# Optimization experiments

Hardware: AMD Instinct MI355X
Metric: run time of the kernel (lower is better)

## Reference

```python
import jax, jax.numpy as jnp
import numpy as np

B, C, T, H, W = 8, 128, 16, 32, 32
M, N, CS = 64, 64, 64


def setup_inputs() -> dict:
    key = jax.random.key(0)
    ks = jax.random.split(key, 12)
    s = 0.02
    return {
        "input": jax.random.normal(ks[0], (B, C, T, H, W), dtype=jnp.float32),
        "condition": jax.random.normal(ks[1], (B, CS), dtype=jnp.float32),
        # 1x1x1 Conv3d weights collapse to (out, in) matrices
        "W_phi": jax.random.normal(ks[2], (M, C), dtype=jnp.float32) * s,
        "b_phi": jax.random.normal(ks[3], (M,), dtype=jnp.float32) * s,
        "W_theta": jax.random.normal(ks[4], (N, C), dtype=jnp.float32) * s,
        "b_theta": jax.random.normal(ks[5], (N,), dtype=jnp.float32) * s,
        "W_rho": jax.random.normal(ks[6], (N, C), dtype=jnp.float32) * s,
        "b_rho": jax.random.normal(ks[7], (N,), dtype=jnp.float32) * s,
        "W1": jax.random.normal(ks[8], (CS, CS), dtype=jnp.float32) * s,
        "b1": jax.random.normal(ks[9], (CS,), dtype=jnp.float32) * s,
        "W2": jax.random.normal(ks[10], (H * W, CS), dtype=jnp.float32) * s,
        "b2": jax.random.normal(ks[11], (H * W,), dtype=jnp.float32) * s,
    }


def _pointwise_conv3d(x, Wt, b):
    # Conv3d with kernel=1, stride=1 == channel mixing
    return jnp.einsum('bcthw,oc->bothw', x, Wt) + b[None, :, None, None, None]


def reference(input, condition, W_phi, b_phi, W_theta, b_theta, W_rho, b_rho, W1, b1, W2, b2):
    x = input.reshape(-1, C, T, H, W)
    cond = condition.reshape(x.shape[0], -1)
    A = _pointwise_conv3d(x, W_phi, b_phi)                       # (b,m,t,h,w)
    B0 = _pointwise_conv3d(x, W_theta, b_theta)                  # (b,n,t,h,w)
    Bm = jax.nn.softmax(B0.reshape(B0.shape[0], B0.shape[1], -1), axis=-1).reshape(B0.shape)
    # FC_Cond: Linear+ReLU, Linear+ReLU, then softmax over h*w
    h1 = jax.nn.relu(cond @ W1.T + b1)
    h2 = jax.nn.relu(h1 @ W2.T + b2)
    Cm = jax.nn.softmax(h2, axis=-1).reshape(-1, H, W)           # (b,h,w)
    BC = Bm * Cm[:, None, None, :, :]                            # (b,n,t,h,w)
    AB_T = jnp.einsum('bmthw,bnthw->bmn', A, BC)                 # (b,m,n)
    V = jax.nn.softmax(_pointwise_conv3d(x, W_rho, b_rho), axis=1)
    Z = jnp.einsum('bmn,bnthw->bmthw', AB_T, V)
    attn = jnp.transpose(Bm * V, (0, 1, 3, 4, 2))                # (b,n,h,w,t)
    return (Z, attn)
```

## Files before the change

### kernel.cpp

```cpp
#include <hip/hip_runtime.h>

#define CC 128
#define SB 16384

typedef _Float16 half2_t __attribute__((ext_vector_type(2)));
typedef _Float16 half4_t __attribute__((ext_vector_type(4)));
typedef _Float16 half8_t __attribute__((ext_vector_type(8)));
typedef float    f32x4  __attribute__((ext_vector_type(4)));

#define WH_OFF   0u
#define ABH_OFF  0u
#define BIAS_OFF 49152u
#define CM_OFF   50176u
#define SUME_OFF 82944u
#define PT_OFF   262144u
#define VT_OFF   33816576u

__global__ void k0_setup(const float* __restrict__ cond,
                         const float* __restrict__ W_phi, const float* __restrict__ b_phi,
                         const float* __restrict__ W_theta, const float* __restrict__ b_theta,
                         const float* __restrict__ W_rho, const float* __restrict__ b_rho,
                         const float* __restrict__ W1, const float* __restrict__ b1,
                         const float* __restrict__ W2, const float* __restrict__ b2,
                         char* __restrict__ wsc) {
  __shared__ float sc[64], sh1[64], red[256];
  int t = threadIdx.x, bid = blockIdx.x;
  if (bid < 8) {
    int b = bid;
    if (t < 64) sc[t] = cond[b*64 + t];
    __syncthreads();
    if (t < 64) {
      float acc = b1[t];
      for (int k = 0; k < 64; ++k) acc += sc[k] * W1[t*64 + k];
      sh1[t] = fmaxf(acc, 0.f);
    }
    __syncthreads();
    float ev[4]; float ps = 0.f;
    #pragma unroll
    for (int q = 0; q < 4; ++q) {
      int o = q*256 + t;
      float acc = b2[o];
      for (int k = 0; k < 64; ++k) acc += sh1[k] * W2[o*64 + k];
      ev[q] = __expf(fmaxf(acc, 0.f));
      ps += ev[q];
    }
    red[t] = ps; __syncthreads();
    for (int s = 128; s > 0; s >>= 1) { if (t < s) red[t] += red[t+s]; __syncthreads(); }
    float inv = 1.f / red[0];
    float* cm = (float*)(wsc + CM_OFF);
    #pragma unroll
    for (int q = 0; q < 4; ++q) cm[b*1024 + q*256 + t] = ev[q] * inv;
  } else {
    int r = bid - 8;
    _Float16* wh = (_Float16*)(wsc + WH_OFF);
    for (int i = r*256 + t; i < 24576; i += 2048) {
      int set = i >> 13, mk = i & 8191;
      const float* W = (set == 0) ? W_phi : (set == 1 ? W_theta : W_rho);
      wh[i] = (_Float16)W[mk];
    }
    if (r == 0 && t < 192) {
      float* bias = (float*)(wsc + BIAS_OFF);
      bias[t] = (t < 64) ? b_phi[t] : (t < 128 ? b_theta[t-64] : b_rho[t-128]);
    }
    if (r == 1) {
      float* se = (float*)(wsc + SUME_OFF);
      for (int i = t; i < 512; i += 256) se[i] = 0.f;
    }
  }
}

__global__ __launch_bounds__(256, 4) void kC_main(
    const float* __restrict__ x, const _Float16* __restrict__ wh,
    const float* __restrict__ bias, const float* __restrict__ cm,
    float* __restrict__ sumE, _Float16* __restrict__ vt,
    char* __restrict__ ptb,
    float* __restrict__ part) {
  __shared__ char smem[35328];
  __shared__ float se_l[256];
  _Float16* Xh  = (_Float16*)smem;
  _Float16* A_l = (_Float16*)smem;
  _Float16* E_l = (_Float16*)(smem + 17408);

  int t = threadIdx.x;
  int lane = t & 63, wv = t >> 6, ln = lane & 15, q = lane >> 4;
  int bid = blockIdx.x, b = bid >> 7, chunk = bid & 127;
  int s0 = chunk * 128;

  const float* xb = x + (size_t)b*CC*SB + s0;
  #pragma unroll
  for (int r = 0; r < 16; ++r) {
    int fid = r*256 + t;
    int c = fid >> 5, s4 = (fid & 31) << 2;
    float4 v = *(const float4*)(xb + (size_t)c*SB + s4);
    half2_t p0 = { (_Float16)v.x, (_Float16)v.y };
    half2_t p1 = { (_Float16)v.z, (_Float16)v.w };
    *(half2_t*)&Xh[c*138 + s4]     = p0;
    *(half2_t*)&Xh[c*138 + s4 + 2] = p1;
  }
  __syncthreads();

  int myp = wv * 32;
  half8_t bf[2][4];
  #pragma unroll
  for (int nt = 0; nt < 2; ++nt) {
    int s = myp + nt*16 + ln;
    #pragma unroll
    for (int kk = 0; kk < 4; ++kk) {
      half8_t h;
      #pragma unroll
      for (int j = 0; j < 8; ++j) h[j] = Xh[(kk*32 + q*8 + j)*138 + s];
      bf[nt][kk] = h;
    }
  }

  int gsl[2] = { s0 + myp + ln, s0 + myp + 16 + ln };
  float cmv[2] = { cm[b*1024 + (gsl[0] & 1023)], cm[b*1024 + (gsl[1] & 1023)] };
  __syncthreads();

  half8_t af[4][4];
  f32x4 d[4][2];
  float ev[4][2][4];

  auto conv = [&](int setoff) {
    #pragma unroll
    for (int mt = 0; mt < 4; ++mt)
      #pragma unroll
      for (int kk = 0; kk < 4; ++kk)
        af[mt][kk] = *(const half8_t*)(wh + setoff + (mt*16 + ln)*128 + kk*32 + q*8);
    #pragma unroll
    for (int mt = 0; mt < 4; ++mt)
      #pragma unroll
      for (int nt = 0; nt < 2; ++nt)
        d[mt][nt] = (f32x4){0.f, 0.f, 0.f, 0.f};
    #pragma unroll
    for (int kk = 0; kk < 4; ++kk)
      #pragma unroll
      for (int mt = 0; mt < 4; ++mt)
        #pragma unroll
        for (int nt = 0; nt < 2; ++nt)
          d[mt][nt] = __builtin_amdgcn_mfma_f32_16x16x32_f16(af[mt][kk], bf[nt][kk],
                                                             d[mt][nt], 0, 0, 0);
  };

  conv(0);
  #pragma unroll
  for (int mt = 0; mt < 4; ++mt) {
    float bv[4]; *(float4*)bv = *(const float4*)(bias + mt*16 + q*4);
    #pragma unroll
    for (int nt = 0; nt < 2; ++nt)
      #pragma unroll
      for (int r = 0; r < 4; ++r)
        A_l[(mt*16 + q*4 + r)*136 + myp + nt*16 + ln] = (_Float16)(d[mt][nt][r] + bv[r]);
  }

  conv(8192);
  float sp[4][4];
  #pragma unroll
  for (int mt = 0; mt < 4; ++mt) {
    float bv[4]; *(float4*)bv = *(const float4*)(bias + 64 + mt*16 + q*4);
    #pragma unroll
    for (int r = 0; r < 4; ++r) {
      #pragma unroll
      for (int nt = 0; nt < 2; ++nt) {
        float e = __expf(d[mt][nt][r] + bv[r]);
        ev[mt][nt][r] = e;
        E_l[(mt*16 + q*4 + r)*136 + myp + nt*16 + ln] = (_Float16)(e * cmv[nt]);
      }
      sp[mt][r] = ev[mt][0][r] + ev[mt][1][r];
    }
  }
  #pragma unroll
  for (int mt = 0; mt < 4; ++mt)
    #pragma unroll
    for (int r = 0; r < 4; ++r) {
      float v = sp[mt][r];
      v += __shfl_xor(v, 1); v += __shfl_xor(v, 2);
      v += __shfl_xor(v, 4); v += __shfl_xor(v, 8);
      sp[mt][r] = v;
    }
  if (ln == 0) {
    #pragma unroll
    for (int mt = 0; mt < 4; ++mt)
      #pragma unroll
      for (int r = 0; r < 4; ++r)
        se_l[wv*64 + mt*16 + q*4 + r] = sp[mt][r];
  }

  conv(16384);
  #pragma unroll
  for (int mt = 0; mt < 4; ++mt) {
    float bv[4]; *(float4*)bv = *(const float4*)(bias + 128 + mt*16 + q*4);
    #pragma unroll
    for (int nt = 0; nt < 2; ++nt)
      #pragma unroll
      for (int r = 0; r < 4; ++r)
        d[mt][nt][r] = __expf(d[mt][nt][r] + bv[r]);
  }
  float cs[2] = {0.f, 0.f};
  #pragma unroll
  for (int mt = 0; mt < 4; ++mt)
    #pragma unroll
    for (int nt = 0; nt < 2; ++nt)
      #pragma unroll
      for (int r = 0; r < 4; ++r) cs[nt] += d[mt][nt][r];
  #pragma unroll
  for (int nt = 0; nt < 2; ++nt) {
    cs[nt] += __shfl_xor(cs[nt], 16);
    cs[nt] += __shfl_xor(cs[nt], 32);
    cs[nt] = 1.f / cs[nt];
  }
  #pragma unroll
  for (int nt = 0; nt < 2; ++nt) {
    size_t grow = (size_t)b*SB + gsl[nt];
    _Float16* vrow = vt + grow*64;
    char* prow = ptb + grow*128;
    #pragma unroll
    for (int mt = 0; mt < 4; ++mt) {
      half4_t hv, hp;
      #pragma unroll
      for (int r = 0; r < 4; ++r) {
        float vv = d[mt][nt][r] * cs[nt];
        hv[r] = (_Float16)vv;
        hp[r] = (_Float16)(vv * ev[mt][nt][r]);
      }
      *(half4_t*)(vrow + mt*16 + q*4) = hv;
      *(half4_t*)(prow + (size_t)(mt*16 + q*4)*2) = hp;
    }
  }
  __syncthreads();

  if (t < 64) {
    float ssum = se_l[t] + se_l[64+t] + se_l[128+t] + se_l[192+t];
    atomicAdd(&sumE[b*64 + t], ssum);
  }

  f32x4 dab[4];
  #pragma unroll
  for (int n2 = 0; n2 < 4; ++n2) dab[n2] = (f32x4){0.f, 0.f, 0.f, 0.f};
  #pragma unroll
  for (int kk = 0; kk < 4; ++kk) {
    half8_t aab = *(half8_t*)&A_l[(wv*16 + ln)*136 + kk*32 + q*8];
    #pragma unroll
    for (int n2 = 0; n2 < 4; ++n2) {
      half8_t bab = *(half8_t*)&E_l[(n2*16 + ln)*136 + kk*32 + q*8];
      dab[n2] = __builtin_amdgcn_mfma_f32_16x16x32_f16(aab, bab, dab[n2], 0, 0, 0);
    }
  }
  float* pp = part + (size_t)bid*4096;
  #pragma unroll
  for (int n2 = 0; n2 < 4; ++n2)
    #pragma unroll
    for (int r = 0; r < 4; ++r)
      pp[(wv*16 + q*4 + r)*64 + n2*16 + ln] = dab[n2][r];
}

__global__ void k2_reduce(const float* __restrict__ part, const float* __restrict__ sumE,
                          _Float16* __restrict__ abh) {
  int idx = blockIdx.x*128 + threadIdx.x;
  int b = idx >> 12, mn = idx & 4095, n = mn & 63;
  const float* p = part + (size_t)b*128*4096 + mn;
  float s = 0.f;
  #pragma unroll 8
  for (int k = 0; k < 128; ++k) s += p[(size_t)k*4096];
  abh[idx] = (_Float16)(s * (1024.f / sumE[b*64 + n]));
}

__global__ __launch_bounds__(256) void k34(const _Float16* __restrict__ abh,
                                           const _Float16* __restrict__ vt,
                                           const char* __restrict__ ptb,
                                           const float* __restrict__ sumE,
                                           float* __restrict__ out) {
  __shared__ _Float16 sm[256*72];
  int t = threadIdx.x;
  if (blockIdx.x < 512) {
    _Float16* Ah = sm;
    int lane = t & 63, wv = t >> 6, ln = lane & 15, q = lane >> 4;
    int bid = blockIdx.x, b = bid >> 6, chunk = bid & 63;
    int s0 = chunk * 256;
    #pragma unroll
    for (int r = 0; r < 2; ++r) {
      int fid = r*256 + t;
      int m = fid >> 3, n8 = fid & 7;
      *(half8_t*)&Ah[m*72 + n8*8] = *(const half8_t*)(abh + b*4096 + m*64 + n8*8);
    }
    __syncthreads();
    half8_t a8[4][2];
    #pragma unroll
    for (int mt = 0; mt < 4; ++mt)
      #pragma unroll
      for (int kk = 0; kk < 2; ++kk)
        a8[mt][kk] = *(half8_t*)&Ah[(mt*16 + ln)*72 + kk*32 + q*8];
    int sw = s0 + wv*64;
    #pragma unroll
    for (int nt = 0; nt < 4; ++nt) {
      int sb = sw + nt*16 + ln;
      const _Float16* vrow = vt + ((size_t)b*SB + sb)*64;
      half8_t b8[2];
      b8[0] = *(const half8_t*)(vrow + q*8);
      b8[1] = *(const half8_t*)(vrow + 32 + q*8);
      f32x4 dz[4];
      #pragma unroll
      for (int mt = 0; mt < 4; ++mt) dz[mt] = (f32x4){0.f, 0.f, 0.f, 0.f};
      #pragma unroll
      for (int kk = 0; kk < 2; ++kk)
        #pragma unroll
        for (int mt = 0; mt < 4; ++mt)
          dz[mt] = __builtin_amdgcn_mfma_f32_16x16x32_f16(a8[mt][kk], b8[kk], dz[mt], 0, 0, 0);
      #pragma unroll
      for (int mt = 0; mt < 4; ++mt)
        #pragma unroll
        for (int r = 0; r < 4; ++r)
          out[((size_t)(b*64 + mt*16 + q*4 + r))*SB + sb] = dz[mt][r] * (1.f/1024.f);
    }
  } else {
    _Float16* P_l = sm;
    int bid = blockIdx.x - 512;
    int b = bid >> 6, hw0 = (bid & 63) * 16;
    int st = t >> 4, h = t & 15;
    int s = st*1024 + hw0 + h;
    const char* prow = ptb + ((size_t)b*SB + s)*128;
    #pragma unroll
    for (int c8 = 0; c8 < 8; ++c8)
      *(half8_t*)&P_l[t*72 + c8*8] = *(const half8_t*)(prow + c8*16);
    __syncthreads();
    int n = t >> 2, oc = t & 3;
    float ri = 1.f / sumE[b*64 + n];
    float* orow = out + 8388608 + (size_t)(b*64 + n)*SB + hw0*16;
    #pragma unroll
    for (int i = 0; i < 16; ++i) {
      int j = oc*64 + i*4;
      int hh = j >> 4, stb = j & 15;
      float w[4];
      #pragma unroll
      for (int r = 0; r < 4; ++r)
        w[r] = (float)P_l[((stb + r)*16 + hh)*72 + n] * ri;
      *(float4*)(orow + j) = *(float4*)w;
    }
  }
}

extern "C" void kernel_launch(void* const* d_in, const int* in_sizes, int n_in,
                              void* d_out, int out_size, void* d_ws, size_t ws_size,
                              hipStream_t stream) {
  const float* input   = (const float*)d_in[0];
  const float* cond    = (const float*)d_in[1];
  const float* W_phi   = (const float*)d_in[2];
  const float* b_phi   = (const float*)d_in[3];
  const float* W_theta = (const float*)d_in[4];
  const float* b_theta = (const float*)d_in[5];
  const float* W_rho   = (const float*)d_in[6];
  const float* b_rho   = (const float*)d_in[7];
  const float* W1      = (const float*)d_in[8];
  const float* b1      = (const float*)d_in[9];
  const float* W2      = (const float*)d_in[10];
  const float* b2      = (const float*)d_in[11];
  char* wsc = (char*)d_ws;
  float* out = (float*)d_out;

  const _Float16* wh = (const _Float16*)(wsc + WH_OFF);
  _Float16* abh  = (_Float16*)(wsc + ABH_OFF);
  const float* bias = (const float*)(wsc + BIAS_OFF);
  const float* cmp  = (const float*)(wsc + CM_OFF);
  float* sumE  = (float*)(wsc + SUME_OFF);
  _Float16* vt = (_Float16*)(wsc + VT_OFF);
  float* part  = out + 8388608;

  hipLaunchKernelGGL(k0_setup, dim3(16), dim3(256), 0, stream,
                     cond, W_phi, b_phi, W_theta, b_theta, W_rho, b_rho,
                     W1, b1, W2, b2, wsc);
  hipLaunchKernelGGL(kC_main, dim3(1024), dim3(256), 0, stream,
                     input, wh, bias, cmp, sumE, vt, (char*)(wsc + PT_OFF), part);
  hipLaunchKernelGGL(k2_reduce, dim3(256), dim3(128), 0, stream, part, sumE, abh);
  hipLaunchKernelGGL(k34, dim3(1024), dim3(256), 0, stream,
                     abh, vt, (const char*)(wsc + PT_OFF), sumE, out);
}
```

Baseline: 211.4 us.

## Replace partial-sum reduce kernel with atomic accumulation and widen main blocks

The main kernel now runs 512 threads per block, each wave handling 16 spatial positions instead of 32, which lowers per-thread register use. The separate k2_reduce pass over per-block partial AB matrices is removed. Each block instead atomically adds its 64x64 partial into a zeroed fp32 buffer, and k34 applies the sumE normalisation and fp16 conversion while loading it. This saves one kernel launch and a large partial-buffer write and read, at the cost of many float atomics on the same addresses and nondeterministic summation order.

```diff
diff --git a/kernel.cpp b/kernel.cpp
--- a/kernel.cpp
+++ b/kernel.cpp
@@ -9,10 +9,10 @@
 typedef float    f32x4  __attribute__((ext_vector_type(4)));
 
 #define WH_OFF   0u
-#define ABH_OFF  0u
 #define BIAS_OFF 49152u
 #define CM_OFF   50176u
 #define SUME_OFF 82944u
+#define AB_OFF   86016u
 #define PT_OFF   262144u
 #define VT_OFF   33816576u
 
@@ -58,6 +58,8 @@
       const float* W = (set == 0) ? W_phi : (set == 1 ? W_theta : W_rho);
       wh[i] = (_Float16)W[mk];
     }
+    float* ab = (float*)(wsc + AB_OFF);
+    for (int i = r*256 + t; i < 32768; i += 2048) ab[i] = 0.f;
     if (r == 0 && t < 192) {
       float* bias = (float*)(wsc + BIAS_OFF);
       bias[t] = (t < 64) ? b_phi[t] : (t < 128 ? b_theta[t-64] : b_rho[t-128]);
@@ -69,14 +71,14 @@
   }
 }
 
-__global__ __launch_bounds__(256, 4) void kC_main(
+__global__ __launch_bounds__(512, 6) void kC_main(
     const float* __restrict__ x, const _Float16* __restrict__ wh,
     const float* __restrict__ bias, const float* __restrict__ cm,
     float* __restrict__ sumE, _Float16* __restrict__ vt,
     char* __restrict__ ptb,
-    float* __restrict__ part) {
+    float* __restrict__ abf) {
   __shared__ char smem[35328];
-  __shared__ float se_l[256];
+  __shared__ float se_l[512];
   _Float16* Xh  = (_Float16*)smem;
   _Float16* A_l = (_Float16*)smem;
   _Float16* E_l = (_Float16*)(smem + 17408);
@@ -88,8 +90,8 @@
 
   const float* xb = x + (size_t)b*CC*SB + s0;
   #pragma unroll
-  for (int r = 0; r < 16; ++r) {
-    int fid = r*256 + t;
+  for (int r = 0; r < 8; ++r) {
+    int fid = r*512 + t;
     int c = fid >> 5, s4 = (fid & 31) << 2;
     float4 v = *(const float4*)(xb + (size_t)c*SB + s4);
     half2_t p0 = { (_Float16)v.x, (_Float16)v.y };
@@ -99,27 +101,22 @@
   }
   __syncthreads();
 
-  int myp = wv * 32;
-  half8_t bf[2][4];
-  #pragma unroll
-  for (int nt = 0; nt < 2; ++nt) {
-    int s = myp + nt*16 + ln;
-    #pragma unroll
-    for (int kk = 0; kk < 4; ++kk) {
-      half8_t h;
-      #pragma unroll
-      for (int j = 0; j < 8; ++j) h[j] = Xh[(kk*32 + q*8 + j)*138 + s];
-      bf[nt][kk] = h;
-    }
-  }
-
-  int gsl[2] = { s0 + myp + ln, s0 + myp + 16 + ln };
-  float cmv[2] = { cm[b*1024 + (gsl[0] & 1023)], cm[b*1024 + (gsl[1] & 1023)] };
+  int myp = wv * 16;
+  half8_t bf[4];
+  #pragma unroll
+  for (int kk = 0; kk < 4; ++kk) {
+    half8_t h;
+    #pragma unroll
+    for (int j = 0; j < 8; ++j) h[j] = Xh[(kk*32 + q*8 + j)*138 + myp + ln];
+    bf[kk] = h;
+  }
+
+  int gs = s0 + myp + ln;
+  float cmv = cm[b*1024 + (gs & 1023)];
   __syncthreads();
 
   half8_t af[4][4];
-  f32x4 d[4][2];
-  float ev[4][2][4];
+  f32x4 d[4];
 
   auto conv = [&](int setoff) {
     #pragma unroll
@@ -129,17 +126,12 @@
         af[mt][kk] = *(const half8_t*)(wh + setoff + (mt*16 + ln)*128 + kk*32 + q*8);
     #pragma unroll
     for (int mt = 0; mt < 4; ++mt)
-      #pragma unroll
-      for (int nt = 0; nt < 2; ++nt)
-        d[mt][nt] = (f32x4){0.f, 0.f, 0.f, 0.f};
+      d[mt] = (f32x4){0.f, 0.f, 0.f, 0.f};
     #pragma unroll
     for (int kk = 0; kk < 4; ++kk)
       #pragma unroll
       for (int mt = 0; mt < 4; ++mt)
-        #pragma unroll
-        for (int nt = 0; nt < 2; ++nt)
-          d[mt][nt] = __builtin_amdgcn_mfma_f32_16x16x32_f16(af[mt][kk], bf[nt][kk],
-                                                             d[mt][nt], 0, 0, 0);
+        d[mt] = __builtin_amdgcn_mfma_f32_16x16x32_f16(af[mt][kk], bf[kk], d[mt], 0, 0, 0);
   };
 
   conv(0);
@@ -147,43 +139,28 @@
   for (int mt = 0; mt < 4; ++mt) {
     float bv[4]; *(float4*)bv = *(const float4*)(bias + mt*16 + q*4);
     #pragma unroll
-    for (int nt = 0; nt < 2; ++nt)
-      #pragma unroll
-      for (int r = 0; r < 4; ++r)
-        A_l[(mt*16 + q*4 + r)*136 + myp + nt*16 + ln] = (_Float16)(d[mt][nt][r] + bv[r]);
+    for (int r = 0; r < 4; ++r)
+      A_l[(mt*16 + q*4 + r)*136 + myp + ln] = (_Float16)(d[mt][r] + bv[r]);
   }
 
   conv(8192);
-  float sp[4][4];
+  float ev[4][4];
   #pragma unroll
   for (int mt = 0; mt < 4; ++mt) {
     float bv[4]; *(float4*)bv = *(const float4*)(bias + 64 + mt*16 + q*4);
     #pragma unroll
     for (int r = 0; r < 4; ++r) {
-      #pragma unroll
-      for (int nt = 0; nt < 2; ++nt) {
-        float e = __expf(d[mt][nt][r] + bv[r]);
-        ev[mt][nt][r] = e;
-        E_l[(mt*16 + q*4 + r)*136 + myp + nt*16 + ln] = (_Float16)(e * cmv[nt]);
-      }
-      sp[mt][r] = ev[mt][0][r] + ev[mt][1][r];
-    }
-  }
-  #pragma unroll
-  for (int mt = 0; mt < 4; ++mt)
+      float e = __expf(d[mt][r] + bv[r]);
+      ev[mt][r] = e;
+      E_l[(mt*16 + q*4 + r)*136 + myp + ln] = (_Float16)(e * cmv);
+    }
     #pragma unroll
     for (int r = 0; r < 4; ++r) {
-      float v = sp[mt][r];
+      float v = ev[mt][r];
       v += __shfl_xor(v, 1); v += __shfl_xor(v, 2);
       v += __shfl_xor(v, 4); v += __shfl_xor(v, 8);
-      sp[mt][r] = v;
-    }
-  if (ln == 0) {
-    #pragma unroll
-    for (int mt = 0; mt < 4; ++mt)
-      #pragma unroll
-      for (int r = 0; r < 4; ++r)
-        se_l[wv*64 + mt*16 + q*4 + r] = sp[mt][r];
+      if (ln == 0) se_l[wv*64 + mt*16 + q*4 + r] = v;
+    }
   }
 
   conv(16384);
@@ -191,27 +168,19 @@
   for (int mt = 0; mt < 4; ++mt) {
     float bv[4]; *(float4*)bv = *(const float4*)(bias + 128 + mt*16 + q*4);
     #pragma unroll
-    for (int nt = 0; nt < 2; ++nt)
-      #pragma unroll
-      for (int r = 0; r < 4; ++r)
-        d[mt][nt][r] = __expf(d[mt][nt][r] + bv[r]);
-  }
-  float cs[2] = {0.f, 0.f};
+    for (int r = 0; r < 4; ++r)
+      d[mt][r] = __expf(d[mt][r] + bv[r]);
+  }
+  float cs = 0.f;
   #pragma unroll
   for (int mt = 0; mt < 4; ++mt)
     #pragma unroll
-    for (int nt = 0; nt < 2; ++nt)
-      #pragma unroll
-      for (int r = 0; r < 4; ++r) cs[nt] += d[mt][nt][r];
-  #pragma unroll
-  for (int nt = 0; nt < 2; ++nt) {
-    cs[nt] += __shfl_xor(cs[nt], 16);
-    cs[nt] += __shfl_xor(cs[nt], 32);
-    cs[nt] = 1.f / cs[nt];
-  }
-  #pragma unroll
-  for (int nt = 0; nt < 2; ++nt) {
-    size_t grow = (size_t)b*SB + gsl[nt];
+    for (int r = 0; r < 4; ++r) cs += d[mt][r];
+  cs += __shfl_xor(cs, 16);
+  cs += __shfl_xor(cs, 32);
+  cs = 1.f / cs;
+  {
+    size_t grow = (size_t)b*SB + gs;
     _Float16* vrow = vt + grow*64;
     char* prow = ptb + grow*128;
     #pragma unroll
@@ -219,9 +188,9 @@
       half4_t hv, hp;
       #pragma unroll
       for (int r = 0; r < 4; ++r) {
-        float vv = d[mt][nt][r] * cs[nt];
+        float vv = d[mt][r] * cs;
         hv[r] = (_Float16)vv;
-        hp[r] = (_Float16)(vv * ev[mt][nt][r]);
+        hp[r] = (_Float16)(vv * ev[mt][r]);
       }
       *(half4_t*)(vrow + mt*16 + q*4) = hv;
       *(half4_t*)(prow + (size_t)(mt*16 + q*4)*2) = hp;
@@ -230,42 +199,34 @@
   __syncthreads();
 
   if (t < 64) {
-    float ssum = se_l[t] + se_l[64+t] + se_l[128+t] + se_l[192+t];
+    float ssum = 0.f;
+    #pragma unroll
+    for (int w = 0; w < 8; ++w) ssum += se_l[w*64 + t];
     atomicAdd(&sumE[b*64 + t], ssum);
   }
 
-  f32x4 dab[4];
-  #pragma unroll
-  for (int n2 = 0; n2 < 4; ++n2) dab[n2] = (f32x4){0.f, 0.f, 0.f, 0.f};
+  int wm = wv & 3, nh = wv >> 2;
+  f32x4 dab[2];
+  dab[0] = (f32x4){0.f, 0.f, 0.f, 0.f};
+  dab[1] = (f32x4){0.f, 0.f, 0.f, 0.f};
   #pragma unroll
   for (int kk = 0; kk < 4; ++kk) {
-    half8_t aab = *(half8_t*)&A_l[(wv*16 + ln)*136 + kk*32 + q*8];
-    #pragma unroll
-    for (int n2 = 0; n2 < 4; ++n2) {
-      half8_t bab = *(half8_t*)&E_l[(n2*16 + ln)*136 + kk*32 + q*8];
-      dab[n2] = __builtin_amdgcn_mfma_f32_16x16x32_f16(aab, bab, dab[n2], 0, 0, 0);
-    }
-  }
-  float* pp = part + (size_t)bid*4096;
-  #pragma unroll
-  for (int n2 = 0; n2 < 4; ++n2)
+    half8_t aab = *(half8_t*)&A_l[(wm*16 + ln)*136 + kk*32 + q*8];
+    #pragma unroll
+    for (int nn = 0; nn < 2; ++nn) {
+      half8_t bab = *(half8_t*)&E_l[((nh*2 + nn)*16 + ln)*136 + kk*32 + q*8];
+      dab[nn] = __builtin_amdgcn_mfma_f32_16x16x32_f16(aab, bab, dab[nn], 0, 0, 0);
+    }
+  }
+  float* ab = abf + b*4096;
+  #pragma unroll
+  for (int nn = 0; nn < 2; ++nn)
     #pragma unroll
     for (int r = 0; r < 4; ++r)
-      pp[(wv*16 + q*4 + r)*64 + n2*16 + ln] = dab[n2][r];
+      atomicAdd(&ab[(wm*16 + q*4 + r)*64 + (nh*2 + nn)*16 + ln], dab[nn][r]);
 }
 
-__global__ void k2_reduce(const float* __restrict__ part, const float* __restrict__ sumE,
-                          _Float16* __restrict__ abh) {
-  int idx = blockIdx.x*128 + threadIdx.x;
-  int b = idx >> 12, mn = idx & 4095, n = mn & 63;
-  const float* p = part + (size_t)b*128*4096 + mn;
-  float s = 0.f;
-  #pragma unroll 8
-  for (int k = 0; k < 128; ++k) s += p[(size_t)k*4096];
-  abh[idx] = (_Float16)(s * (1024.f / sumE[b*64 + n]));
-}
-
-__global__ __launch_bounds__(256) void k34(const _Float16* __restrict__ abh,
+__global__ __launch_bounds__(256) void k34(const float* __restrict__ abf,
                                            const _Float16* __restrict__ vt,
                                            const char* __restrict__ ptb,
                                            const float* __restrict__ sumE,
@@ -277,11 +238,13 @@
     int lane = t & 63, wv = t >> 6, ln = lane & 15, q = lane >> 4;
     int bid = blockIdx.x, b = bid >> 6, chunk = bid & 63;
     int s0 = chunk * 256;
-    #pragma unroll
-    for (int r = 0; r < 2; ++r) {
-      int fid = r*256 + t;
-      int m = fid >> 3, n8 = fid & 7;
-      *(half8_t*)&Ah[m*72 + n8*8] = *(const half8_t*)(abh + b*4096 + m*64 + n8*8);
+    const float* ab = abf + b*4096;
+    const float* se = sumE + b*64;
+    #pragma unroll
+    for (int r = 0; r < 16; ++r) {
+      int idx = r*256 + t;
+      int m = idx >> 6, n = idx & 63;
+      Ah[m*72 + n] = (_Float16)(ab[idx] * (1024.f / se[n]));
     }
     __syncthreads();
     half8_t a8[4][2];
@@ -358,19 +321,17 @@
   float* out = (float*)d_out;
 
   const _Float16* wh = (const _Float16*)(wsc + WH_OFF);
-  _Float16* abh  = (_Float16*)(wsc + ABH_OFF);
   const float* bias = (const float*)(wsc + BIAS_OFF);
   const float* cmp  = (const float*)(wsc + CM_OFF);
   float* sumE  = (float*)(wsc + SUME_OFF);
+  float* abf   = (float*)(wsc + AB_OFF);
   _Float16* vt = (_Float16*)(wsc + VT_OFF);
-  float* part  = out + 8388608;
 
   hipLaunchKernelGGL(k0_setup, dim3(16), dim3(256), 0, stream,
                      cond, W_phi, b_phi, W_theta, b_theta, W_rho, b_rho,
                      W1, b1, W2, b2, wsc);
-  hipLaunchKernelGGL(kC_main, dim3(1024), dim3(256), 0, stream,
-                     input, wh, bias, cmp, sumE, vt, (char*)(wsc + PT_OFF), part);
-  hipLaunchKernelGGL(k2_reduce, dim3(256), dim3(128), 0, stream, part, sumE, abh);
+  hipLaunchKernelGGL(kC_main, dim3(1024), dim3(512), 0, stream,
+                     input, wh, bias, cmp, sumE, vt, (char*)(wsc + PT_OFF), abf);
   hipLaunchKernelGGL(k34, dim3(1024), dim3(256), 0, stream,
-                     abh, vt, (const char*)(wsc + PT_OFF), sumE, out);
+                     abf, vt, (const char*)(wsc + PT_OFF), sumE, out);
 }
```

New measurement: 227.7 us. 7.7% more time.

## Replace partial-sum buffer and reduce kernel with atomic accumulation of AB

Applied to the files above, without the earlier changes.

The main kernel now accumulates its per-block AB^T partial products straight into a zeroed fp32 buffer using atomicAdd. This removes the partial-result writes and the separate k2_reduce launch. The scaling by 1/sumE and the fp16 conversion move into the Z-producing blocks of k34. The attention-transpose blocks are also split into smaller tiles (1536 blocks, less shared memory), and the launch bounds change for kC_main and k34. The cost is heavy atomic contention, with 128 blocks per batch adding into the same 4096 floats, plus a redundant per-block rescale of AB.

```diff
diff --git a/kernel.cpp b/kernel.cpp
--- a/kernel.cpp
+++ b/kernel.cpp
@@ -9,10 +9,10 @@
 typedef float    f32x4  __attribute__((ext_vector_type(4)));
 
 #define WH_OFF   0u
-#define ABH_OFF  0u
 #define BIAS_OFF 49152u
 #define CM_OFF   50176u
 #define SUME_OFF 82944u
+#define AB_OFF   86016u
 #define PT_OFF   262144u
 #define VT_OFF   33816576u
 
@@ -58,6 +58,8 @@
       const float* W = (set == 0) ? W_phi : (set == 1 ? W_theta : W_rho);
       wh[i] = (_Float16)W[mk];
     }
+    float* ab = (float*)(wsc + AB_OFF);
+    for (int i = r*256 + t; i < 32768; i += 2048) ab[i] = 0.f;
     if (r == 0 && t < 192) {
       float* bias = (float*)(wsc + BIAS_OFF);
       bias[t] = (t < 64) ? b_phi[t] : (t < 128 ? b_theta[t-64] : b_rho[t-128]);
@@ -69,12 +71,12 @@
   }
 }
 
-__global__ __launch_bounds__(256, 4) void kC_main(
+__global__ __launch_bounds__(256, 2) void kC_main(
     const float* __restrict__ x, const _Float16* __restrict__ wh,
     const float* __restrict__ bias, const float* __restrict__ cm,
     float* __restrict__ sumE, _Float16* __restrict__ vt,
     char* __restrict__ ptb,
-    float* __restrict__ part) {
+    float* __restrict__ abf) {
   __shared__ char smem[35328];
   __shared__ float se_l[256];
   _Float16* Xh  = (_Float16*)smem;
@@ -246,42 +248,33 @@
       dab[n2] = __builtin_amdgcn_mfma_f32_16x16x32_f16(aab, bab, dab[n2], 0, 0, 0);
     }
   }
-  float* pp = part + (size_t)bid*4096;
+  float* ab = abf + b*4096;
   #pragma unroll
   for (int n2 = 0; n2 < 4; ++n2)
     #pragma unroll
     for (int r = 0; r < 4; ++r)
-      pp[(wv*16 + q*4 + r)*64 + n2*16 + ln] = dab[n2][r];
+      atomicAdd(&ab[(wv*16 + q*4 + r)*64 + n2*16 + ln], dab[n2][r]);
 }
 
-__global__ void k2_reduce(const float* __restrict__ part, const float* __restrict__ sumE,
-                          _Float16* __restrict__ abh) {
-  int idx = blockIdx.x*128 + threadIdx.x;
-  int b = idx >> 12, mn = idx & 4095, n = mn & 63;
-  const float* p = part + (size_t)b*128*4096 + mn;
-  float s = 0.f;
-  #pragma unroll 8
-  for (int k = 0; k < 128; ++k) s += p[(size_t)k*4096];
-  abh[idx] = (_Float16)(s * (1024.f / sumE[b*64 + n]));
-}
-
-__global__ __launch_bounds__(256) void k34(const _Float16* __restrict__ abh,
-                                           const _Float16* __restrict__ vt,
-                                           const char* __restrict__ ptb,
-                                           const float* __restrict__ sumE,
-                                           float* __restrict__ out) {
-  __shared__ _Float16 sm[256*72];
+__global__ __launch_bounds__(256, 6) void k34(const float* __restrict__ abf,
+                                              const _Float16* __restrict__ vt,
+                                              const char* __restrict__ ptb,
+                                              const float* __restrict__ sumE,
+                                              float* __restrict__ out) {
+  __shared__ _Float16 sm[8704];
   int t = threadIdx.x;
   if (blockIdx.x < 512) {
     _Float16* Ah = sm;
     int lane = t & 63, wv = t >> 6, ln = lane & 15, q = lane >> 4;
     int bid = blockIdx.x, b = bid >> 6, chunk = bid & 63;
     int s0 = chunk * 256;
-    #pragma unroll
-    for (int r = 0; r < 2; ++r) {
-      int fid = r*256 + t;
-      int m = fid >> 3, n8 = fid & 7;
-      *(half8_t*)&Ah[m*72 + n8*8] = *(const half8_t*)(abh + b*4096 + m*64 + n8*8);
+    const float* ab = abf + b*4096;
+    const float* se = sumE + b*64;
+    #pragma unroll
+    for (int r = 0; r < 16; ++r) {
+      int idx = r*256 + t;
+      int m = idx >> 6, n = idx & 63;
+      Ah[m*72 + n] = (_Float16)(ab[idx] * (1024.f / se[n]));
     }
     __syncthreads();
     half8_t a8[4][2];
@@ -314,26 +307,29 @@
     }
   } else {
     _Float16* P_l = sm;
-    int bid = blockIdx.x - 512;
-    int b = bid >> 6, hw0 = (bid & 63) * 16;
-    int st = t >> 4, h = t & 15;
-    int s = st*1024 + hw0 + h;
-    const char* prow = ptb + ((size_t)b*SB + s)*128;
-    #pragma unroll
-    for (int c8 = 0; c8 < 8; ++c8)
-      *(half8_t*)&P_l[t*72 + c8*8] = *(const half8_t*)(prow + c8*16);
+    int a = blockIdx.x - 512;
+    int b = a >> 7, hw0 = (a & 127) * 8;
+    {
+      int rp = t >> 1, half = t & 1;
+      int s = (rp >> 3)*1024 + hw0 + (rp & 7);
+      const char* prow = ptb + ((size_t)b*SB + s)*128 + half*64;
+      _Float16* dst = &P_l[rp*68 + half*32];
+      #pragma unroll
+      for (int c8 = 0; c8 < 4; ++c8)
+        *(half8_t*)(dst + c8*8) = *(const half8_t*)(prow + c8*16);
+    }
     __syncthreads();
     int n = t >> 2, oc = t & 3;
     float ri = 1.f / sumE[b*64 + n];
     float* orow = out + 8388608 + (size_t)(b*64 + n)*SB + hw0*16;
     #pragma unroll
-    for (int i = 0; i < 16; ++i) {
-      int j = oc*64 + i*4;
-      int hh = j >> 4, stb = j & 15;
+    for (int i = 0; i < 8; ++i) {
+      int j = oc*32 + i*4;
+      int h = j >> 4, tt = j & 15;
       float w[4];
       #pragma unroll
       for (int r = 0; r < 4; ++r)
-        w[r] = (float)P_l[((stb + r)*16 + hh)*72 + n] * ri;
+        w[r] = (float)P_l[((tt + r)*8 + h)*68 + n] * ri;
       *(float4*)(orow + j) = *(float4*)w;
     }
   }
@@ -358,19 +354,17 @@
   float* out = (float*)d_out;
 
   const _Float16* wh = (const _Float16*)(wsc + WH_OFF);
-  _Float16* abh  = (_Float16*)(wsc + ABH_OFF);
   const float* bias = (const float*)(wsc + BIAS_OFF);
   const float* cmp  = (const float*)(wsc + CM_OFF);
   float* sumE  = (float*)(wsc + SUME_OFF);
+  float* abf   = (float*)(wsc + AB_OFF);
   _Float16* vt = (_Float16*)(wsc + VT_OFF);
-  float* part  = out + 8388608;
 
   hipLaunchKernelGGL(k0_setup, dim3(16), dim3(256), 0, stream,
                      cond, W_phi, b_phi, W_theta, b_theta, W_rho, b_rho,
                      W1, b1, W2, b2, wsc);
   hipLaunchKernelGGL(kC_main, dim3(1024), dim3(256), 0, stream,
-                     input, wh, bias, cmp, sumE, vt, (char*)(wsc + PT_OFF), part);
-  hipLaunchKernelGGL(k2_reduce, dim3(256), dim3(128), 0, stream, part, sumE, abh);
-  hipLaunchKernelGGL(k34, dim3(1024), dim3(256), 0, stream,
-                     abh, vt, (const char*)(wsc + PT_OFF), sumE, out);
+                     input, wh, bias, cmp, sumE, vt, (char*)(wsc + PT_OFF), abf);
+  hipLaunchKernelGGL(k34, dim3(1536), dim3(256), 0, stream,
+                     abf, vt, (const char*)(wsc + PT_OFF), sumE, out);
 }
```

Result: slower. 225.5 us (+6.7%).
